# Performance work log

Hardware: AMD Instinct MI355X
Metric: run time of the kernel (lower is better)

Reference implementation:

```python
import jax, jax.numpy as jnp
import numpy as np

N_HEADS = 16
ROPE_BASE = 10000.0


def _rotate_half(x):
    x1, x2 = jnp.split(x, 2, axis=-1)
    return jnp.concatenate([-x2, x1], axis=-1)


def _rope_cos_sin(positions, d_k, dtype):
    # standard YaRN-style rotary tables (attention scale mscale = 1.0)
    inv_freq = 1.0 / (ROPE_BASE ** (jnp.arange(0, d_k, 2, dtype=jnp.float32) / d_k))
    freqs = positions.astype(jnp.float32)[:, None] * inv_freq[None, :]  # [T, d_k/2]
    emb = jnp.concatenate([freqs, freqs], axis=-1)                      # [T, d_k]
    return jnp.cos(emb).astype(dtype), jnp.sin(emb).astype(dtype)


def setup_inputs() -> dict:
    key = jax.random.key(0)
    ks = jax.random.split(key, 8)
    B, T, D = 1, 2048, 1024
    s = 0.02
    return {
        "query": jax.random.normal(ks[0], (B, T, D), jnp.float32),
        "key": jax.random.normal(ks[1], (B, T, D), jnp.float32),
        "value": jax.random.normal(ks[2], (B, T, D), jnp.float32),
        "yarn_positions": jnp.arange(T, dtype=jnp.int32),
        "wq": jax.random.normal(ks[3], (D, D), jnp.float32) * s,
        "wk": jax.random.normal(ks[4], (D, D), jnp.float32) * s,
        "wv": jax.random.normal(ks[5], (D, D), jnp.float32) * s,
        "wo_w": jax.random.normal(ks[6], (D, D), jnp.float32) * s,
        "wo_b": jnp.zeros((D,), jnp.float32),
    }


def reference(query, key, value, yarn_positions, wq, wk, wv, wo_w, wo_b):
    B, Tq, D = query.shape
    Tk = key.shape[1]
    H = N_HEADS
    dk = D // H

    # nn.Linear(bias=False): y = x @ W.T
    Q = (query @ wq.T).reshape(B, Tq, H, dk).transpose(0, 2, 1, 3)  # [B,H,Tq,dk]
    K = (key @ wk.T).reshape(B, Tk, H, dk).transpose(0, 2, 1, 3)
    V = (value @ wv.T).reshape(B, Tk, H, dk).transpose(0, 2, 1, 3)

    # YaRN rotary position embedding on Q and K (same positions for q and k)
    cos, sin = _rope_cos_sin(yarn_positions, dk, Q.dtype)  # [T, dk]
    cos = cos[None, None, :, :]
    sin = sin[None, None, :, :]
    Q = Q * cos + _rotate_half(Q) * sin
    K = K * cos + _rotate_half(K) * sin

    scale = 1.0 / jnp.sqrt(jnp.asarray(dk, Q.dtype))
    scores = jnp.einsum('bhqd,bhkd->bhqk', Q, K) * scale  # [B,H,Tq,Tk]

    # causal mask (is_causal=True)
    causal = jnp.triu(jnp.ones((Tq, Tk), dtype=bool), 1)
    scores = jnp.where(causal[None, None], -jnp.inf, scores)

    attn = jax.nn.softmax(scores, axis=-1)
    out = jnp.einsum('bhqk,bhkd->bhqd', attn, V)
    out = out.transpose(0, 2, 1, 3).reshape(B, Tq, D)
    return out @ wo_w.T + wo_b
```

## Files before the change

### kernel.cpp

```cpp
#include <hip/hip_runtime.h>
#include <hip/hip_bf16.h>
#include <stdint.h>

#define TT 2048
#define DD 1024
#define NH 16
#define DK 64

typedef __attribute__((ext_vector_type(8))) short bf16x8;
typedef __attribute__((ext_vector_type(4))) float f32x4;
typedef __attribute__((ext_vector_type(8))) unsigned short u16x8;
typedef __attribute__((ext_vector_type(4))) unsigned short u16x4;

__device__ __forceinline__ unsigned short f2bf(float f) {
  union { float f; unsigned u; } x; x.f = f;
  unsigned r = (x.u + 0x7FFFu + ((x.u >> 16) & 1u)) >> 16;
  return (unsigned short)r;
}

__device__ __forceinline__ void gload16(const void* g, void* l) {
  __builtin_amdgcn_global_load_lds(
      (const __attribute__((address_space(1))) unsigned int*)g,
      (__attribute__((address_space(3))) unsigned int*)l, 16, 0, 0);
}

__global__ __launch_bounds__(256) void cvt_all(
    const float* __restrict__ q, const float* __restrict__ k, const float* __restrict__ v,
    const float* __restrict__ wq, const float* __restrict__ wk, const float* __restrict__ wv,
    const float* __restrict__ wo,
    unsigned short* __restrict__ oq, unsigned short* __restrict__ ok, unsigned short* __restrict__ ov,
    unsigned short* __restrict__ owq, unsigned short* __restrict__ owk, unsigned short* __restrict__ owv,
    unsigned short* __restrict__ owo,
    const int* __restrict__ pos, float* __restrict__ cosT, float* __restrict__ sinT) {
  int b = blockIdx.x;
  if (b >= 5120) {
    int idx = (b - 5120) * 256 + threadIdx.x;
    int t = idx >> 5, i = idx & 31;
    float inv = exp2f((float)i * -0.41524101186092028f);
    float ang = (float)pos[t] * inv;
    cosT[idx] = cosf(ang);
    sinT[idx] = sinf(ang);
    return;
  }
  const float* src; unsigned short* dst; int sb;
  if (b < 1024)      { src = q;  dst = oq;  sb = b; }
  else if (b < 2048) { src = k;  dst = ok;  sb = b - 1024; }
  else if (b < 3072) { src = v;  dst = ov;  sb = b - 2048; }
  else if (b < 3584) { src = wq; dst = owq; sb = b - 3072; }
  else if (b < 4096) { src = wk; dst = owk; sb = b - 3584; }
  else if (b < 4608) { src = wv; dst = owv; sb = b - 4096; }
  else               { src = wo; dst = owo; sb = b - 4608; }
  size_t i0 = (size_t)sb * 2048 + (size_t)threadIdx.x * 8;
  f32x4 a = *(const f32x4*)(src + i0);
  f32x4 c = *(const f32x4*)(src + i0 + 4);
  u16x8 r;
#pragma unroll
  for (int j = 0; j < 4; ++j) { r[j] = f2bf(a[j]); r[j + 4] = f2bf(c[j]); }
  *(u16x8*)(dst + i0) = r;
}

__global__ __launch_bounds__(256) void gemm_qkv(
    const unsigned short* __restrict__ xq, const unsigned short* __restrict__ xk,
    const unsigned short* __restrict__ xv,
    const unsigned short* __restrict__ wqb, const unsigned short* __restrict__ wkb,
    const unsigned short* __restrict__ wvb,
    unsigned short* __restrict__ QF, unsigned short* __restrict__ KF,
    unsigned short* __restrict__ VF,
    const float* __restrict__ cosT, const float* __restrict__ sinT) {
  __shared__ unsigned short Ash[64 * 64];
  __shared__ unsigned short Bsh[128 * 64];
  const int z = blockIdx.z;
  const unsigned short* A = (z == 0) ? xq : (z == 1) ? xk : xv;
  const unsigned short* W = (z == 0) ? wqb : (z == 1) ? wkb : wvb;
  const int brow = blockIdx.x * 64;
  const int bcol = blockIdx.y * 128;
  const int tid = threadIdx.x;
  const int lane = tid & 63;
  const int w = tid >> 6;
  const int wr = w >> 1, wc = w & 1;
  const char* Ab = (const char*)A + (size_t)brow * (DD * 2);
  const char* Wb = (const char*)W + (size_t)bcol * (DD * 2);
  char* AshB = (char*)Ash;
  char* BshB = (char*)Bsh;
  f32x4 acc[2][4];
#pragma unroll
  for (int mi = 0; mi < 2; ++mi)
#pragma unroll
    for (int ni = 0; ni < 4; ++ni)
#pragma unroll
      for (int r = 0; r < 4; ++r) acc[mi][ni][r] = 0.0f;

  for (int k0 = 0; k0 < DD; k0 += 64) {
    __syncthreads();
#pragma unroll
    for (int it = 0; it < 2; ++it) {
      int c = it * 256 + tid;
      int row = c >> 3;
      int xb = (c & 7) << 4;
      int sxb = xb ^ ((row & 7) << 4);
      int ldso = (it * 256 + (tid & 192)) << 4;
      gload16(Ab + (size_t)row * (DD * 2) + k0 * 2 + sxb, AshB + ldso);
    }
#pragma unroll
    for (int it = 0; it < 4; ++it) {
      int c = it * 256 + tid;
      int row = c >> 3;
      int xb = (c & 7) << 4;
      int sxb = xb ^ ((row & 7) << 4);
      int ldso = (it * 256 + (tid & 192)) << 4;
      gload16(Wb + (size_t)row * (DD * 2) + k0 * 2 + sxb, BshB + ldso);
    }
    __syncthreads();
#pragma unroll
    for (int ks = 0; ks < 2; ++ks) {
      bf16x8 af[2], bfr[4];
      int colb = ks * 64 + ((lane >> 4) << 4);
#pragma unroll
      for (int mi = 0; mi < 2; ++mi) {
        int row = wr * 32 + mi * 16 + (lane & 15);
        af[mi] = *(const bf16x8*)(AshB + row * 128 + (colb ^ ((row & 7) << 4)));
      }
#pragma unroll
      for (int ni = 0; ni < 4; ++ni) {
        int row = wc * 64 + ni * 16 + (lane & 15);
        bfr[ni] = *(const bf16x8*)(BshB + row * 128 + (colb ^ ((row & 7) << 4)));
      }
#pragma unroll
      for (int mi = 0; mi < 2; ++mi)
#pragma unroll
        for (int ni = 0; ni < 4; ++ni)
          acc[mi][ni] = __builtin_amdgcn_mfma_f32_16x16x32_bf16(af[mi], bfr[ni], acc[mi][ni], 0, 0, 0);
    }
  }

  const int hcol = bcol + wc * 64;
  const int h = hcol >> 6;
  if (z == 0) {
    const float sc = 0.18033688011112042f;
#pragma unroll
    for (int mi = 0; mi < 2; ++mi) {
#pragma unroll
      for (int r = 0; r < 4; ++r) {
        int t = brow + wr * 32 + mi * 16 + ((lane >> 4) << 2) + r;
        int qw_ = t >> 5, mif = (t >> 4) & 1, r16 = t & 15;
        size_t fb = (((size_t)(h * 64 + qw_) * 2 + mif) * 2) * 1024;
#pragma unroll
        for (int ni = 0; ni < 2; ++ni) {
          int dl = ni * 16 + (lane & 15);
          float cv = cosT[t * 32 + dl];
          float sv = sinT[t * 32 + dl];
          float x1 = acc[mi][ni][r];
          float x2 = acc[mi][ni + 2][r];
          size_t off = fb + (size_t)(r16 + 16 * (dl >> 3)) * 16 + (dl & 7) * 2;
          *(unsigned short*)((char*)QF + off) = f2bf((x1 * cv - x2 * sv) * sc);
          *(unsigned short*)((char*)QF + off + 1024) = f2bf((x2 * cv + x1 * sv) * sc);
        }
      }
    }
  } else if (z == 1) {
#pragma unroll
    for (int mi = 0; mi < 2; ++mi) {
#pragma unroll
      for (int r = 0; r < 4; ++r) {
        int t = brow + wr * 32 + mi * 16 + ((lane >> 4) << 2) + r;
        int kt = t >> 6, nif = (t >> 4) & 3, r16 = t & 15;
        size_t fb = (((size_t)(h * 32 + kt) * 2) * 4 + nif) * 1024;
#pragma unroll
        for (int ni = 0; ni < 2; ++ni) {
          int dl = ni * 16 + (lane & 15);
          float cv = cosT[t * 32 + dl];
          float sv = sinT[t * 32 + dl];
          float x1 = acc[mi][ni][r];
          float x2 = acc[mi][ni + 2][r];
          size_t off = fb + (size_t)(r16 + 16 * (dl >> 3)) * 16 + (dl & 7) * 2;
          *(unsigned short*)((char*)KF + off) = f2bf(x1 * cv - x2 * sv);
          *(unsigned short*)((char*)KF + off + 4096) = f2bf(x2 * cv + x1 * sv);
        }
      }
    }
  } else {
#pragma unroll
    for (int mi = 0; mi < 2; ++mi) {
      int t0 = brow + wr * 32 + mi * 16 + ((lane >> 4) << 2);
      int kt = t0 >> 6, ksf = (t0 & 63) >> 5, slot = (t0 & 31) >> 3, j0 = t0 & 7;
#pragma unroll
      for (int ni = 0; ni < 4; ++ni) {
        int dh = ni * 16 + (lane & 15);
        int lanef = (dh & 15) + 16 * slot;
        size_t off = ((((size_t)(h * 32 + kt) * 2 + ksf) * 4 + ni) * 64 + lanef) * 16 + j0 * 2;
        u16x4 pk;
#pragma unroll
        for (int r = 0; r < 4; ++r) pk[r] = f2bf(acc[mi][ni][r]);
        *(u16x4*)((char*)VF + off) = pk;
      }
    }
  }
}

__global__ __launch_bounds__(256, 2) void attn_fa(
    const unsigned short* __restrict__ QF, const unsigned short* __restrict__ KF,
    const unsigned short* __restrict__ VF, unsigned short* __restrict__ AO) {
  __shared__ char LB[26624];
  __shared__ float MR[4][32];
  const int tid = threadIdx.x;
  const int lane = tid & 63;
  const int w = tid >> 6;
  const int bid = blockIdx.x;
  const int xcd = bid & 7;
  const int idx = bid >> 3;
  const int h = xcd * 2 + (idx & 1);
  const int qw = 63 - (idx >> 1);
  const int q0w = qw * 32;
  const int NT = (qw >> 1) + 1;
  char* PshB = LB + w * 4096;
  const char* Kb = (const char*)KF + (size_t)h * 32 * 8192;
  const char* Vb = (const char*)VF + (size_t)h * 32 * 8192;

  bf16x8 qf[2][2];
  {
    const char* Qb = (const char*)QF + (size_t)(h * 64 + qw) * 4096;
#pragma unroll
    for (int mi = 0; mi < 2; ++mi)
#pragma unroll
      for (int ks = 0; ks < 2; ++ks)
        qf[mi][ks] = *(const bf16x8*)(Qb + (mi * 2 + ks) * 1024 + lane * 16);
  }

  bf16x8 vone;
#pragma unroll
  for (int j = 0; j < 8; ++j) vone[j] = (short)0x3F80;

  f32x4 accO[2][5];
  float mrow[2];
#pragma unroll
  for (int mi = 0; mi < 2; ++mi) {
    mrow[mi] = -1e30f;
#pragma unroll
    for (int ni = 0; ni < 5; ++ni)
#pragma unroll
      for (int r = 0; r < 4; ++r) accO[mi][ni][r] = 0.0f;
  }

  bf16x8 kfA[2][4], kfB[2][4], vf[2][4];
  {
    int kt0 = (w < NT) ? w : 0;
    const char* p = Kb + (size_t)kt0 * 8192 + lane * 16;
#pragma unroll
    for (int ks = 0; ks < 2; ++ks)
#pragma unroll
      for (int ni = 0; ni < 4; ++ni)
        kfA[ks][ni] = *(const bf16x8*)(p + (ks * 4 + ni) * 1024);
  }

  for (int kt = w; kt < NT; kt += 4) {
    {
      const char* p = Vb + (size_t)kt * 8192 + lane * 16;
#pragma unroll
      for (int ks = 0; ks < 2; ++ks)
#pragma unroll
        for (int ni = 0; ni < 4; ++ni)
          vf[ks][ni] = *(const bf16x8*)(p + (ks * 4 + ni) * 1024);
    }
    f32x4 s[2][4];
#pragma unroll
    for (int mi = 0; mi < 2; ++mi)
#pragma unroll
      for (int ni = 0; ni < 4; ++ni)
#pragma unroll
        for (int r = 0; r < 4; ++r) s[mi][ni][r] = 0.0f;
    __builtin_amdgcn_s_setprio(1);
#pragma unroll
    for (int ks = 0; ks < 2; ++ks)
#pragma unroll
      for (int mi = 0; mi < 2; ++mi)
#pragma unroll
        for (int ni = 0; ni < 4; ++ni)
          s[mi][ni] = __builtin_amdgcn_mfma_f32_16x16x32_bf16(kfA[ks][ni], qf[mi][ks], s[mi][ni], 0, 0, 0);
    __builtin_amdgcn_s_setprio(0);
    if (kt + 4 < NT) {
      const char* p = Kb + (size_t)(kt + 4) * 8192 + lane * 16;
#pragma unroll
      for (int ks = 0; ks < 2; ++ks)
#pragma unroll
        for (int ni = 0; ni < 4; ++ni)
          kfB[ks][ni] = *(const bf16x8*)(p + (ks * 4 + ni) * 1024);
    }

    if (kt == NT - 1) {
#pragma unroll
      for (int mi = 0; mi < 2; ++mi) {
        int qq = q0w + mi * 16 + (lane & 15);
#pragma unroll
        for (int ni = 0; ni < 4; ++ni) {
          int kb = kt * 64 + ni * 16 + ((lane >> 4) << 2);
#pragma unroll
          for (int r = 0; r < 4; ++r)
            if (kb + r > qq) s[mi][ni][r] = -1e30f;
        }
      }
    }
    float rmx[2];
#pragma unroll
    for (int mi = 0; mi < 2; ++mi) {
      f32x4 t;
#pragma unroll
      for (int r = 0; r < 4; ++r)
        t[r] = fmaxf(fmaxf(s[mi][0][r], s[mi][1][r]), fmaxf(s[mi][2][r], s[mi][3][r]));
      float mx = fmaxf(fmaxf(t[0], t[1]), fmaxf(t[2], t[3]));
      mx = fmaxf(mx, __shfl_xor(mx, 16, 64));
      mx = fmaxf(mx, __shfl_xor(mx, 32, 64));
      rmx[mi] = mx;
    }
    bool need = (rmx[0] > mrow[0] + 8.0f) || (rmx[1] > mrow[1] + 8.0f);
    if (__any(need)) {
#pragma unroll
      for (int mi = 0; mi < 2; ++mi) {
        float mn = fmaxf(mrow[mi], rmx[mi]);
        float al = exp2f(mrow[mi] - mn);
        mrow[mi] = mn;
        float ar[4];
#pragma unroll
        for (int r = 0; r < 4; ++r) ar[r] = __shfl(al, ((lane >> 4) << 2) + r, 64);
#pragma unroll
        for (int ni = 0; ni < 5; ++ni)
#pragma unroll
          for (int r = 0; r < 4; ++r) accO[mi][ni][r] *= ar[r];
      }
    }
#pragma unroll
    for (int mi = 0; mi < 2; ++mi) {
      int row = mi * 16 + (lane & 15);
      int rbase = row * 128;
      int sw = (row & 7) << 4;
#pragma unroll
      for (int ni = 0; ni < 4; ++ni) {
        unsigned u0 = __float_as_uint(exp2f(s[mi][ni][0] - mrow[mi]));
        unsigned u1 = __float_as_uint(exp2f(s[mi][ni][1] - mrow[mi]));
        unsigned u2 = __float_as_uint(exp2f(s[mi][ni][2] - mrow[mi]));
        unsigned u3 = __float_as_uint(exp2f(s[mi][ni][3] - mrow[mi]));
        uint2 pk;
        pk.x = (u0 >> 16) | (u1 & 0xFFFF0000u);
        pk.y = (u2 >> 16) | (u3 & 0xFFFF0000u);
        int cb = ni * 32 + ((lane >> 4) << 3);
        *(uint2*)(PshB + rbase + (cb ^ sw)) = pk;
      }
    }
    asm volatile("" ::: "memory");
    __builtin_amdgcn_s_setprio(1);
#pragma unroll
    for (int ks = 0; ks < 2; ++ks) {
      bf16x8 pf[2];
#pragma unroll
      for (int mi = 0; mi < 2; ++mi) {
        int row = mi * 16 + (lane & 15);
        int cb = ks * 64 + ((lane >> 4) << 4);
        pf[mi] = *(const bf16x8*)(PshB + row * 128 + (cb ^ ((row & 7) << 4)));
      }
#pragma unroll
      for (int mi = 0; mi < 2; ++mi) {
#pragma unroll
        for (int ni = 0; ni < 4; ++ni)
          accO[mi][ni] = __builtin_amdgcn_mfma_f32_16x16x32_bf16(pf[mi], vf[ks][ni], accO[mi][ni], 0, 0, 0);
        accO[mi][4] = __builtin_amdgcn_mfma_f32_16x16x32_bf16(pf[mi], vone, accO[mi][4], 0, 0, 0);
      }
    }
    __builtin_amdgcn_s_setprio(0);
#pragma unroll
    for (int ks = 0; ks < 2; ++ks)
#pragma unroll
      for (int ni = 0; ni < 4; ++ni) kfA[ks][ni] = kfB[ks][ni];
  }

  __syncthreads();
  if ((lane >> 4) == 0) {
    MR[w][lane] = mrow[0];
    MR[w][16 + lane] = mrow[1];
  }
  if (w > 0) {
    float* MOw = (float*)LB + (size_t)(w - 1) * 32 * 68;
#pragma unroll
    for (int mi = 0; mi < 2; ++mi) {
#pragma unroll
      for (int r = 0; r < 4; ++r) {
        int rq = mi * 16 + ((lane >> 4) << 2) + r;
#pragma unroll
        for (int ni = 0; ni < 4; ++ni)
          MOw[rq * 68 + ni * 16 + (lane & 15)] = accO[mi][ni][r];
        if ((lane & 15) == 0) MOw[rq * 68 + 64] = accO[mi][4][r];
      }
    }
  }
  __syncthreads();
  if (w == 0) {
    const float* MOp = (const float*)LB;
#pragma unroll
    for (int mi = 0; mi < 2; ++mi) {
#pragma unroll
      for (int r = 0; r < 4; ++r) {
        int rq = mi * 16 + ((lane >> 4) << 2) + r;
        float m0 = MR[0][rq], m1 = MR[1][rq], m2 = MR[2][rq], m3 = MR[3][rq];
        float M = fmaxf(fmaxf(m0, m1), fmaxf(m2, m3));
        float a0 = exp2f(m0 - M), a1 = exp2f(m1 - M);
        float a2 = exp2f(m2 - M), a3 = exp2f(m3 - M);
        float denom = a0 * accO[mi][4][r] + a1 * MOp[(0 * 32 + rq) * 68 + 64] +
                      a2 * MOp[(1 * 32 + rq) * 68 + 64] + a3 * MOp[(2 * 32 + rq) * 68 + 64];
        float inv = 1.0f / denom;
        int t = q0w + rq;
#pragma unroll
        for (int ni = 0; ni < 4; ++ni) {
          int dh = ni * 16 + (lane & 15);
          float o = a0 * accO[mi][ni][r] + a1 * MOp[(0 * 32 + rq) * 68 + dh] +
                    a2 * MOp[(1 * 32 + rq) * 68 + dh] + a3 * MOp[(2 * 32 + rq) * 68 + dh];
          AO[(size_t)t * DD + h * DK + dh] = f2bf(o * inv);
        }
      }
    }
  }
}

__global__ __launch_bounds__(256) void gemm_o(
    const unsigned short* __restrict__ A, const unsigned short* __restrict__ W,
    const float* __restrict__ bias, float* __restrict__ out) {
  __shared__ unsigned short Ash[128 * 64];
  __shared__ unsigned short Bsh[64 * 64];
  const int brow = blockIdx.x * 128;
  const int bcol = blockIdx.y * 64;
  const int tid = threadIdx.x;
  const int lane = tid & 63;
  const int w = tid >> 6;
  const char* Ab = (const char*)A + (size_t)brow * (DD * 2);
  const char* Wb = (const char*)W + (size_t)bcol * (DD * 2);
  char* AshB = (char*)Ash;
  char* BshB = (char*)Bsh;
  f32x4 acc[2][4];
#pragma unroll
  for (int mi = 0; mi < 2; ++mi)
#pragma unroll
    for (int ni = 0; ni < 4; ++ni)
#pragma unroll
      for (int r = 0; r < 4; ++r) acc[mi][ni][r] = 0.0f;

  for (int k0 = 0; k0 < DD; k0 += 64) {
    __syncthreads();
#pragma unroll
    for (int it = 0; it < 4; ++it) {
      int c = it * 256 + tid;
      int row = c >> 3;
      int xb = (c & 7) << 4;
      int sxb = xb ^ ((row & 7) << 4);
      int ldso = (it * 256 + (tid & 192)) << 4;
      gload16(Ab + (size_t)row * (DD * 2) + k0 * 2 + sxb, AshB + ldso);
    }
#pragma unroll
    for (int it = 0; it < 2; ++it) {
      int c = it * 256 + tid;
      int row = c >> 3;
      int xb = (c & 7) << 4;
      int sxb = xb ^ ((row & 7) << 4);
      int ldso = (it * 256 + (tid & 192)) << 4;
      gload16(Wb + (size_t)row * (DD * 2) + k0 * 2 + sxb, BshB + ldso);
    }
    __syncthreads();
#pragma unroll
    for (int ks = 0; ks < 2; ++ks) {
      bf16x8 af[2], bfr[4];
      int colb = ks * 64 + ((lane >> 4) << 4);
#pragma unroll
      for (int mi = 0; mi < 2; ++mi) {
        int row = w * 32 + mi * 16 + (lane & 15);
        af[mi] = *(const bf16x8*)(AshB + row * 128 + (colb ^ ((row & 7) << 4)));
      }
#pragma unroll
      for (int ni = 0; ni < 4; ++ni) {
        int row = ni * 16 + (lane & 15);
        bfr[ni] = *(const bf16x8*)(BshB + row * 128 + (colb ^ ((row & 7) << 4)));
      }
#pragma unroll
      for (int mi = 0; mi < 2; ++mi)
#pragma unroll
        for (int ni = 0; ni < 4; ++ni)
          acc[mi][ni] = __builtin_amdgcn_mfma_f32_16x16x32_bf16(af[mi], bfr[ni], acc[mi][ni], 0, 0, 0);
    }
  }
#pragma unroll
  for (int mi = 0; mi < 2; ++mi)
#pragma unroll
    for (int r = 0; r < 4; ++r) {
      int t = brow + w * 32 + mi * 16 + ((lane >> 4) << 2) + r;
#pragma unroll
      for (int ni = 0; ni < 4; ++ni) {
        int o = bcol + ni * 16 + (lane & 15);
        out[(size_t)t * DD + o] = acc[mi][ni][r] + bias[o];
      }
    }
}

extern "C" void kernel_launch(void* const* d_in, const int* in_sizes, int n_in,
                              void* d_out, int out_size, void* d_ws, size_t ws_size,
                              hipStream_t stream) {
  const float* q  = (const float*)d_in[0];
  const float* k  = (const float*)d_in[1];
  const float* v  = (const float*)d_in[2];
  const int* pos  = (const int*)d_in[3];
  const float* wq = (const float*)d_in[4];
  const float* wk = (const float*)d_in[5];
  const float* wv = (const float*)d_in[6];
  const float* wo = (const float*)d_in[7];
  const float* wob = (const float*)d_in[8];
  float* out = (float*)d_out;
  char* ws = (char*)d_ws;

  const size_t MB = 1u << 20;
  unsigned short* XQ = (unsigned short*)(ws + 0 * MB);
  unsigned short* XK = (unsigned short*)(ws + 4 * MB);
  unsigned short* XV = (unsigned short*)(ws + 8 * MB);
  unsigned short* WQ = (unsigned short*)(ws + 12 * MB);
  unsigned short* WK = (unsigned short*)(ws + 14 * MB);
  unsigned short* WV = (unsigned short*)(ws + 16 * MB);
  unsigned short* WO = (unsigned short*)(ws + 18 * MB);
  unsigned short* QF = (unsigned short*)(ws + 20 * MB);
  unsigned short* KF = (unsigned short*)(ws + 24 * MB);
  unsigned short* VF = (unsigned short*)(ws + 28 * MB);
  unsigned short* AOb = (unsigned short*)(ws + 32 * MB);
  float* COS = (float*)(ws + 36 * MB);
  float* SIN = (float*)(ws + 36 * MB + 262144);

  hipLaunchKernelGGL(cvt_all, dim3(5376), dim3(256), 0, stream,
                     q, k, v, wq, wk, wv, wo, XQ, XK, XV, WQ, WK, WV, WO,
                     pos, COS, SIN);
  hipLaunchKernelGGL(gemm_qkv, dim3(32, 8, 3), dim3(256), 0, stream,
                     XQ, XK, XV, WQ, WK, WV, QF, KF, VF, COS, SIN);
  hipLaunchKernelGGL(attn_fa, dim3(1024), dim3(256), 0, stream, QF, KF, VF, AOb);
  hipLaunchKernelGGL(gemm_o, dim3(16, 16), dim3(256), 0, stream, AOb, WO, wob, out);
}
```

Measured before the change: 71.84 us.

## Double-buffer LDS tiles in QKV and output GEMMs; shrink output GEMM tile

```diff
diff --git a/kernel.cpp b/kernel.cpp
--- a/kernel.cpp
+++ b/kernel.cpp
@@ -67,8 +67,8 @@
     unsigned short* __restrict__ QF, unsigned short* __restrict__ KF,
     unsigned short* __restrict__ VF,
     const float* __restrict__ cosT, const float* __restrict__ sinT) {
-  __shared__ unsigned short Ash[64 * 64];
-  __shared__ unsigned short Bsh[128 * 64];
+  __shared__ unsigned short Ash[2][64 * 64];
+  __shared__ unsigned short Bsh[2][128 * 64];
   const int z = blockIdx.z;
   const unsigned short* A = (z == 0) ? xq : (z == 1) ? xk : xv;
   const unsigned short* W = (z == 0) ? wqb : (z == 1) ? wkb : wvb;
@@ -90,8 +90,7 @@
 #pragma unroll
       for (int r = 0; r < 4; ++r) acc[mi][ni][r] = 0.0f;
 
-  for (int k0 = 0; k0 < DD; k0 += 64) {
-    __syncthreads();
+  auto STAGE = [&](int k0, int buf) {
 #pragma unroll
     for (int it = 0; it < 2; ++it) {
       int c = it * 256 + tid;
@@ -99,7 +98,7 @@
       int xb = (c & 7) << 4;
       int sxb = xb ^ ((row & 7) << 4);
       int ldso = (it * 256 + (tid & 192)) << 4;
-      gload16(Ab + (size_t)row * (DD * 2) + k0 * 2 + sxb, AshB + ldso);
+      gload16(Ab + (size_t)row * (DD * 2) + k0 * 2 + sxb, AshB + buf * 8192 + ldso);
     }
 #pragma unroll
     for (int it = 0; it < 4; ++it) {
@@ -108,9 +107,19 @@
       int xb = (c & 7) << 4;
       int sxb = xb ^ ((row & 7) << 4);
       int ldso = (it * 256 + (tid & 192)) << 4;
-      gload16(Wb + (size_t)row * (DD * 2) + k0 * 2 + sxb, BshB + ldso);
-    }
-    __syncthreads();
+      gload16(Wb + (size_t)row * (DD * 2) + k0 * 2 + sxb, BshB + buf * 16384 + ldso);
+    }
+  };
+
+  STAGE(0, 0);
+  asm volatile("s_waitcnt vmcnt(0)" ::: "memory");
+  __syncthreads();
+  int cur = 0;
+
+  for (int kt = 0; kt < 16; ++kt) {
+    if (kt + 1 < 16) STAGE((kt + 1) * 64, cur ^ 1);
+    const char* Ac = AshB + cur * 8192;
+    const char* Bc = BshB + cur * 16384;
 #pragma unroll
     for (int ks = 0; ks < 2; ++ks) {
       bf16x8 af[2], bfr[4];
@@ -118,12 +127,12 @@
 #pragma unroll
       for (int mi = 0; mi < 2; ++mi) {
         int row = wr * 32 + mi * 16 + (lane & 15);
-        af[mi] = *(const bf16x8*)(AshB + row * 128 + (colb ^ ((row & 7) << 4)));
+        af[mi] = *(const bf16x8*)(Ac + row * 128 + (colb ^ ((row & 7) << 4)));
       }
 #pragma unroll
       for (int ni = 0; ni < 4; ++ni) {
         int row = wc * 64 + ni * 16 + (lane & 15);
-        bfr[ni] = *(const bf16x8*)(BshB + row * 128 + (colb ^ ((row & 7) << 4)));
+        bfr[ni] = *(const bf16x8*)(Bc + row * 128 + (colb ^ ((row & 7) << 4)));
       }
 #pragma unroll
       for (int mi = 0; mi < 2; ++mi)
@@ -131,6 +140,9 @@
         for (int ni = 0; ni < 4; ++ni)
           acc[mi][ni] = __builtin_amdgcn_mfma_f32_16x16x32_bf16(af[mi], bfr[ni], acc[mi][ni], 0, 0, 0);
     }
+    asm volatile("s_waitcnt vmcnt(0)" ::: "memory");
+    __syncthreads();
+    cur ^= 1;
   }
 
   const int hcol = bcol + wc * 64;
@@ -258,7 +270,7 @@
 #pragma unroll
       for (int ks = 0; ks < 2; ++ks)
 #pragma unroll
-        for (int ni = 0; ni < 4; ++ni)
+      for (int ni = 0; ni < 4; ++ni)
           vf[ks][ni] = *(const bf16x8*)(p + (ks * 4 + ni) * 1024);
     }
     f32x4 s[2][4];
@@ -421,36 +433,27 @@
 __global__ __launch_bounds__(256) void gemm_o(
     const unsigned short* __restrict__ A, const unsigned short* __restrict__ W,
     const float* __restrict__ bias, float* __restrict__ out) {
-  __shared__ unsigned short Ash[128 * 64];
-  __shared__ unsigned short Bsh[64 * 64];
-  const int brow = blockIdx.x * 128;
+  __shared__ unsigned short Ash[2][64 * 64];
+  __shared__ unsigned short Bsh[2][64 * 64];
+  const int brow = blockIdx.x * 64;
   const int bcol = blockIdx.y * 64;
   const int tid = threadIdx.x;
   const int lane = tid & 63;
   const int w = tid >> 6;
+  const int wr = w >> 1, wc = w & 1;
   const char* Ab = (const char*)A + (size_t)brow * (DD * 2);
   const char* Wb = (const char*)W + (size_t)bcol * (DD * 2);
   char* AshB = (char*)Ash;
   char* BshB = (char*)Bsh;
-  f32x4 acc[2][4];
+  f32x4 acc[2][2];
 #pragma unroll
   for (int mi = 0; mi < 2; ++mi)
 #pragma unroll
-    for (int ni = 0; ni < 4; ++ni)
+    for (int ni = 0; ni < 2; ++ni)
 #pragma unroll
       for (int r = 0; r < 4; ++r) acc[mi][ni][r] = 0.0f;
 
-  for (int k0 = 0; k0 < DD; k0 += 64) {
-    __syncthreads();
-#pragma unroll
-    for (int it = 0; it < 4; ++it) {
-      int c = it * 256 + tid;
-      int row = c >> 3;
-      int xb = (c & 7) << 4;
-      int sxb = xb ^ ((row & 7) << 4);
-      int ldso = (it * 256 + (tid & 192)) << 4;
-      gload16(Ab + (size_t)row * (DD * 2) + k0 * 2 + sxb, AshB + ldso);
-    }
+  auto STAGE = [&](int k0, int buf) {
 #pragma unroll
     for (int it = 0; it < 2; ++it) {
       int c = it * 256 + tid;
@@ -458,38 +461,52 @@
       int xb = (c & 7) << 4;
       int sxb = xb ^ ((row & 7) << 4);
       int ldso = (it * 256 + (tid & 192)) << 4;
-      gload16(Wb + (size_t)row * (DD * 2) + k0 * 2 + sxb, BshB + ldso);
-    }
+      gload16(Ab + (size_t)row * (DD * 2) + k0 * 2 + sxb, AshB + buf * 8192 + ldso);
+      gload16(Wb + (size_t)row * (DD * 2) + k0 * 2 + sxb, BshB + buf * 8192 + ldso);
+    }
+  };
+
+  STAGE(0, 0);
+  asm volatile("s_waitcnt vmcnt(0)" ::: "memory");
+  __syncthreads();
+  int cur = 0;
+
+  for (int kt = 0; kt < 16; ++kt) {
+    if (kt + 1 < 16) STAGE((kt + 1) * 64, cur ^ 1);
+    const char* Ac = AshB + cur * 8192;
+    const char* Bc = BshB + cur * 8192;
+#pragma unroll
+    for (int ks = 0; ks < 2; ++ks) {
+      bf16x8 af[2], bfr[2];
+      int colb = ks * 64 + ((lane >> 4) << 4);
+#pragma unroll
+      for (int mi = 0; mi < 2; ++mi) {
+        int row = wr * 32 + mi * 16 + (lane & 15);
+        af[mi] = *(const bf16x8*)(Ac + row * 128 + (colb ^ ((row & 7) << 4)));
+      }
+#pragma unroll
+      for (int ni = 0; ni < 2; ++ni) {
+        int row = wc * 32 + ni * 16 + (lane & 15);
+        bfr[ni] = *(const bf16x8*)(Bc + row * 128 + (colb ^ ((row & 7) << 4)));
+      }
+#pragma unroll
+      for (int mi = 0; mi < 2; ++mi)
+#pragma unroll
+        for (int ni = 0; ni < 2; ++ni)
+          acc[mi][ni] = __builtin_amdgcn_mfma_f32_16x16x32_bf16(af[mi], bfr[ni], acc[mi][ni], 0, 0, 0);
+    }
+    asm volatile("s_waitcnt vmcnt(0)" ::: "memory");
     __syncthreads();
-#pragma unroll
-    for (int ks = 0; ks < 2; ++ks) {
-      bf16x8 af[2], bfr[4];
-      int colb = ks * 64 + ((lane >> 4) << 4);
-#pragma unroll
-      for (int mi = 0; mi < 2; ++mi) {
-        int row = w * 32 + mi * 16 + (lane & 15);
-        af[mi] = *(const bf16x8*)(AshB + row * 128 + (colb ^ ((row & 7) << 4)));
-      }
-#pragma unroll
-      for (int ni = 0; ni < 4; ++ni) {
-        int row = ni * 16 + (lane & 15);
-        bfr[ni] = *(const bf16x8*)(BshB + row * 128 + (colb ^ ((row & 7) << 4)));
-      }
-#pragma unroll
-      for (int mi = 0; mi < 2; ++mi)
-#pragma unroll
-        for (int ni = 0; ni < 4; ++ni)
-          acc[mi][ni] = __builtin_amdgcn_mfma_f32_16x16x32_bf16(af[mi], bfr[ni], acc[mi][ni], 0, 0, 0);
-    }
+    cur ^= 1;
   }
 #pragma unroll
   for (int mi = 0; mi < 2; ++mi)
 #pragma unroll
     for (int r = 0; r < 4; ++r) {
-      int t = brow + w * 32 + mi * 16 + ((lane >> 4) << 2) + r;
-#pragma unroll
-      for (int ni = 0; ni < 4; ++ni) {
-        int o = bcol + ni * 16 + (lane & 15);
+      int t = brow + wr * 32 + mi * 16 + ((lane >> 4) << 2) + r;
+#pragma unroll
+      for (int ni = 0; ni < 2; ++ni) {
+        int o = bcol + wc * 32 + ni * 16 + (lane & 15);
         out[(size_t)t * DD + o] = acc[mi][ni][r] + bias[o];
       }
     }
@@ -531,5 +548,5 @@
   hipLaunchKernelGGL(gemm_qkv, dim3(32, 8, 3), dim3(256), 0, stream,
                      XQ, XK, XV, WQ, WK, WV, QF, KF, VF, COS, SIN);
   hipLaunchKernelGGL(attn_fa, dim3(1024), dim3(256), 0, stream, QF, KF, VF, AOb);
-  hipLaunchKernelGGL(gemm_o, dim3(16, 16), dim3(256), 0, stream, AOb, WO, wob, out);
-}
+  hipLaunchKernelGGL(gemm_o, dim3(32, 16), dim3(256), 0, stream, AOb, WO, wob, out);
+}
```

Result: no change. 71.46 us (-0.5%).
